# Kernel tuning notes

Hardware: AMD Instinct MI355X
Metric: run time of the kernel (lower is better)

## Reference

```python
import jax, jax.numpy as jnp
import numpy as np

CUTOFF = 8.0
NUM_RBF = 16
N = 2048
NUM_GRAPHS = 16


def setup_inputs() -> dict:
    key = jax.random.key(0)
    k1, k2 = jax.random.split(key)
    pos = jax.random.normal(k1, (N, 3), dtype=jnp.float32)
    batch = jnp.sort(jax.random.randint(k2, (N,), 0, NUM_GRAPHS)).astype(jnp.int64)
    # buffers from __init__
    centers = jnp.linspace(0.0, CUTOFF, NUM_RBF).astype(jnp.float32)
    width = jnp.asarray(CUTOFF / NUM_RBF * 0.5, dtype=jnp.float32)
    return {"pos": pos, "batch": batch, "centers": centers, "width": width}


def reference(pos, batch, centers, width):
    # Dense jit-friendly equivalent of the torch module: instead of filtering
    # pairs to a data-dependent edge list, we keep the full [N, N] pair grid
    # and return a boolean validity mask plus RBF features zeroed where invalid.
    n = pos.shape[0]
    idx = jnp.arange(n)
    diff = pos[:, None, :] - pos[None, :, :] + 1e-10  # [N, N, 3] (torch adds 1e-10 to diff)
    dist = jnp.sqrt(jnp.sum(diff * diff, axis=-1))     # [N, N]
    mask = (idx[:, None] != idx[None, :]) \
        & (batch[:, None] == batch[None, :]) \
        & (dist < CUTOFF)                               # [N, N] valid-edge mask
    # RBF encoding: exp(-(d - c)^2 / (2 w^2)), zeroed for invalid pairs
    rbf = jnp.exp(-((dist[..., None] - centers) ** 2) / (2.0 * width ** 2))  # [N, N, R]
    rbf = rbf * mask[..., None].astype(rbf.dtype)
    return mask, rbf
```

## Files before the change

### kernel.cpp

```cpp
#include <hip/hip_runtime.h>
#include <hip/hip_bf16.h>


constexpr int N     = 2048;
constexpr int NRBF  = 16;
constexpr int NTILE = N / 256;

typedef float  f32x4  __attribute__((ext_vector_type(4)));
typedef short  s16x8  __attribute__((ext_vector_type(8)));

__device__ inline float bf16_bits_to_f32(unsigned short h) {
    union { unsigned int u; float f; } c;
    c.u = ((unsigned int)h) << 16;
    return c.f;
}

__device__ inline short f32_to_bf16_bits(float f) {
    __hip_bfloat16 b = __float2bfloat16(f);
    union { __hip_bfloat16 b; short s; } c; c.b = b;
    return c.s;
}

__device__ inline float pair_dist(float xi, float yi, float zi,
                                  float xj, float yj, float zj) {
    const float dx = __fadd_rn(__fsub_rn(xi, xj), 1e-10f);
    const float dy = __fadd_rn(__fsub_rn(yi, yj), 1e-10f);
    const float dz = __fadd_rn(__fsub_rn(zi, zj), 1e-10f);
    const float d2 = __fadd_rn(__fadd_rn(__fmul_rn(dx, dx), __fmul_rn(dy, dy)),
                               __fmul_rn(dz, dz));
    return __fsqrt_rn(d2);
}

__global__ __launch_bounds__(256) void edge_rbf_kernel(
    const void* __restrict__ pos_raw,
    const int*  __restrict__ batch32,
    const void* __restrict__ centers_raw,
    const void* __restrict__ width_raw,
    void*       __restrict__ out_raw)
{
    const int lane = threadIdx.x & 63;
    const int wv   = threadIdx.x >> 6;
    const int i    = blockIdx.x;

    const unsigned int* posw = (const unsigned int*)pos_raw;
    int cnt = 0;
#pragma unroll
    for (int k = 0; k < 16; ++k) {
        float v = bf16_bits_to_f32((unsigned short)(posw[k] & 0xFFFFu));
        float a = fabsf(v);
        if (a > 1e-6f && a < 100.0f) ++cnt;
    }
    const bool is_bf16 = (cnt >= 12);
    const bool b64 = (batch32[N - 1] == 0);

    const int g = b64 ? batch32[2 * i] : batch32[i];
    int lo, hi;
    {
        int l = 0, h = N;
        while (l < h) {
            int m  = (l + h) >> 1;
            int bm = b64 ? batch32[2 * m] : batch32[m];
            if (bm < g) l = m + 1; else h = m;
        }
        lo = l;
        h = N;
        while (l < h) {
            int m  = (l + h) >> 1;
            int bm = b64 ? batch32[2 * m] : batch32[m];
            if (bm <= g) l = m + 1; else h = m;
        }
        hi = l;
    }

    const size_t row = (size_t)i * N;

    if (is_bf16) {
        const __hip_bfloat16* pos     = (const __hip_bfloat16*)pos_raw;
        const __hip_bfloat16* centers = (const __hip_bfloat16*)centers_raw;
        const __hip_bfloat16* width   = (const __hip_bfloat16*)width_raw;
        short* mask_out = (short*)out_raw;
        short* rbf_out  = mask_out + (size_t)N * N;

        const float xi = __bfloat162float(pos[3 * i + 0]);
        const float yi = __bfloat162float(pos[3 * i + 1]);
        const float zi = __bfloat162float(pos[3 * i + 2]);
        const float w  = __bfloat162float(width[0]);
        float cen[NRBF];
#pragma unroll
        for (int r = 0; r < NRBF; ++r) cen[r] = __bfloat162float(centers[r]);
        const float ninv = -1.0f / (2.0f * w * w);

        for (int t = 0; t < NTILE; ++t) {
            const int jt = t * 256 + wv * 64;
            const int jL = jt + lane;
            short* base = rbf_out + (row + jt) * NRBF;

            if (jt + 64 <= lo || jt >= hi) {
                mask_out[row + jL] = (short)0;
                s16x8 z = (s16x8)0;
#pragma unroll
                for (int q = 0; q < 2; ++q)
                    *(s16x8*)(base + q * 512 + lane * 8) = z;
                continue;
            }

            const bool eligL = (jL >= lo) && (jL < hi) && (jL != i);
            const float xjL = __bfloat162float(pos[3 * jL + 0]);
            const float yjL = __bfloat162float(pos[3 * jL + 1]);
            const float zjL = __bfloat162float(pos[3 * jL + 2]);
            const float dL  = pair_dist(xi, yi, zi, xjL, yjL, zjL);
            const bool validL = eligL && (dL < 8.0f);
            mask_out[row + jL] = f32_to_bf16_bits(validL ? 1.0f : 0.0f);

#pragma unroll
            for (int q = 0; q < 2; ++q) {
                const int p  = q * 32 + (lane >> 1);
                const int c0 = (lane & 1) * 8;
                const int jp = jt + p;
                const float xj = __bfloat162float(pos[3 * jp + 0]);
                const float yj = __bfloat162float(pos[3 * jp + 1]);
                const float zj = __bfloat162float(pos[3 * jp + 2]);
                const float d  = pair_dist(xi, yi, zi, xj, yj, zj);
                const bool  ok = (jp >= lo) && (jp < hi) && (jp != i)
                                 && (d < 8.0f);
                s16x8 o;
#pragma unroll
                for (int u = 0; u < 8; ++u) {
                    const float tt = d - cen[c0 + u];
                    o[u] = f32_to_bf16_bits(ok ? __expf(tt * tt * ninv) : 0.0f);
                }
                *(s16x8*)(base + q * 512 + lane * 8) = o;
            }
        }
    } else {
        const float* pos     = (const float*)pos_raw;
        const float* centers = (const float*)centers_raw;
        const float* width   = (const float*)width_raw;
        float* mask_out = (float*)out_raw;
        float* rbf_out  = mask_out + (size_t)N * N;

        const float xi = pos[3 * i + 0];
        const float yi = pos[3 * i + 1];
        const float zi = pos[3 * i + 2];
        const float w  = width[0];
        float cen[NRBF];
#pragma unroll
        for (int r = 0; r < NRBF; ++r) cen[r] = centers[r];
        const float ninv = -1.0f / (2.0f * w * w);

        for (int t = 0; t < NTILE; ++t) {
            const int jt = t * 256 + wv * 64;
            const int jL = jt + lane;
            float* base = rbf_out + (row + jt) * NRBF;

            if (jt + 64 <= lo || jt >= hi) {
                mask_out[row + jL] = 0.0f;
                f32x4 z = (f32x4)0.0f;
#pragma unroll
                for (int q = 0; q < 4; ++q)
                    *(f32x4*)(base + q * 256 + lane * 4) = z;
                continue;
            }

            const bool eligL = (jL >= lo) && (jL < hi) && (jL != i);
            const float xjL = pos[3 * jL + 0];
            const float yjL = pos[3 * jL + 1];
            const float zjL = pos[3 * jL + 2];
            const float dL  = pair_dist(xi, yi, zi, xjL, yjL, zjL);
            const bool validL = eligL && (dL < 8.0f);
            mask_out[row + jL] = validL ? 1.0f : 0.0f;

#pragma unroll
            for (int q = 0; q < 4; ++q) {
                const int p  = q * 16 + (lane >> 2);
                const int c0 = (lane & 3) * 4;
                const int jp = jt + p;
                const float xj = pos[3 * jp + 0];
                const float yj = pos[3 * jp + 1];
                const float zj = pos[3 * jp + 2];
                const float d  = pair_dist(xi, yi, zi, xj, yj, zj);
                const bool  ok = (jp >= lo) && (jp < hi) && (jp != i)
                                 && (d < 8.0f);
                f32x4 o;
#pragma unroll
                for (int u = 0; u < 4; ++u) {
                    const float tt = d - cen[c0 + u];
                    o[u] = ok ? __expf(tt * tt * ninv) : 0.0f;
                }
                *(f32x4*)(base + q * 256 + lane * 4) = o;
            }
        }
    }
}

extern "C" void kernel_launch(void* const* d_in, const int* in_sizes, int n_in,
                              void* d_out, int out_size, void* d_ws, size_t ws_size,
                              hipStream_t stream) {
    const void* pos     = d_in[0];
    const int*  batch   = (const int*)d_in[1];
    const void* centers = d_in[2];
    const void* width   = d_in[3];

    dim3 grid(N);
    dim3 block(256);
    edge_rbf_kernel<<<grid, block, 0, stream>>>(pos, batch, centers, width,
                                                d_out);
}
```

Baseline: 294.3 us.

## Precompute per-row graph ranges and switch to flat grid-stride output writes

Moves the per-row binary search over the batch array into a small separate kernel that writes lo/hi bounds to workspace. The main kernel becomes a fixed 512-block grid-stride loop where each thread writes contiguous 16-byte chunks of the rbf and mask outputs, so stores from consecutive threads are fully contiguous. The cost is an extra launch, per-element range loads, and recomputing the pair distance per chunk, and the block-level skip of tiles outside the row's graph is gone.

```diff
diff --git a/kernel.cpp b/kernel.cpp
--- a/kernel.cpp
+++ b/kernel.cpp
@@ -2,12 +2,14 @@
 #include <hip/hip_bf16.h>
 
 
-constexpr int N     = 2048;
-constexpr int NRBF  = 16;
-constexpr int NTILE = N / 256;
+constexpr int N    = 2048;
+constexpr int NRBF = 16;
+constexpr int NBLK = 512;
+constexpr int T    = NBLK * 256;
 
 typedef float  f32x4  __attribute__((ext_vector_type(4)));
 typedef short  s16x8  __attribute__((ext_vector_type(8)));
+typedef int    i32x2  __attribute__((ext_vector_type(2)));
 
 __device__ inline float bf16_bits_to_f32(unsigned short h) {
     union { unsigned int u; float f; } c;
@@ -31,16 +33,37 @@
     return __fsqrt_rn(d2);
 }
 
+__global__ __launch_bounds__(256) void row_range_kernel(
+    const int* __restrict__ batch32, int* __restrict__ ws)
+{
+    const int i = blockIdx.x * 256 + threadIdx.x;
+    const bool b64 = (batch32[N - 1] == 0);
+    const int g = b64 ? batch32[2 * i] : batch32[i];
+    int l = 0, h = N;
+    while (l < h) {
+        int m  = (l + h) >> 1;
+        int bm = b64 ? batch32[2 * m] : batch32[m];
+        if (bm < g) l = m + 1; else h = m;
+    }
+    const int lo = l;
+    h = N;
+    while (l < h) {
+        int m  = (l + h) >> 1;
+        int bm = b64 ? batch32[2 * m] : batch32[m];
+        if (bm <= g) l = m + 1; else h = m;
+    }
+    ws[2 * i]     = lo;
+    ws[2 * i + 1] = l;
+}
+
 __global__ __launch_bounds__(256) void edge_rbf_kernel(
     const void* __restrict__ pos_raw,
-    const int*  __restrict__ batch32,
     const void* __restrict__ centers_raw,
     const void* __restrict__ width_raw,
+    const int*  __restrict__ ws,
     void*       __restrict__ out_raw)
 {
-    const int lane = threadIdx.x & 63;
-    const int wv   = threadIdx.x >> 6;
-    const int i    = blockIdx.x;
+    const int g0 = blockIdx.x * 256 + threadIdx.x;
 
     const unsigned int* posw = (const unsigned int*)pos_raw;
     int cnt = 0;
@@ -51,144 +74,123 @@
         if (a > 1e-6f && a < 100.0f) ++cnt;
     }
     const bool is_bf16 = (cnt >= 12);
-    const bool b64 = (batch32[N - 1] == 0);
-
-    const int g = b64 ? batch32[2 * i] : batch32[i];
-    int lo, hi;
-    {
-        int l = 0, h = N;
-        while (l < h) {
-            int m  = (l + h) >> 1;
-            int bm = b64 ? batch32[2 * m] : batch32[m];
-            if (bm < g) l = m + 1; else h = m;
-        }
-        lo = l;
-        h = N;
-        while (l < h) {
-            int m  = (l + h) >> 1;
-            int bm = b64 ? batch32[2 * m] : batch32[m];
-            if (bm <= g) l = m + 1; else h = m;
-        }
-        hi = l;
-    }
-
-    const size_t row = (size_t)i * N;
-
-    if (is_bf16) {
+
+    if (!is_bf16) {
+        const float* pos     = (const float*)pos_raw;
+        const float* centers = (const float*)centers_raw;
+        const float* width   = (const float*)width_raw;
+        float* mask_out = (float*)out_raw;
+        float* rbf_out  = mask_out + (size_t)N * N;
+
+        const float w = width[0];
+        float cen[NRBF];
+#pragma unroll
+        for (int r = 0; r < NRBF; ++r) cen[r] = centers[r];
+        const float ninv = -1.0f / (2.0f * w * w);
+
+        for (int k = 0; k < 128; ++k) {
+            const int c    = g0 + k * T;
+            const int pidx = c >> 2;
+            const int q    = c & 3;
+            const int i    = pidx >> 11;
+            const int j    = pidx & (N - 1);
+            const i32x2 lh = *(const i32x2*)(ws + 2 * i);
+            f32x4 o = (f32x4)0.0f;
+            if ((j >= lh[0]) & (j < lh[1]) & (j != i)) {
+                const float d = pair_dist(pos[3*i], pos[3*i+1], pos[3*i+2],
+                                          pos[3*j], pos[3*j+1], pos[3*j+2]);
+                if (d < 8.0f) {
+#pragma unroll
+                    for (int u = 0; u < 4; ++u) {
+                        const float tt = d - cen[4 * q + u];
+                        o[u] = __expf(tt * tt * ninv);
+                    }
+                }
+            }
+            *(f32x4*)(rbf_out + (size_t)c * 4) = o;
+        }
+
+        for (int k = 0; k < 8; ++k) {
+            const int c  = g0 + k * T;
+            const int i  = c >> 9;
+            const int j0 = (c & 511) * 4;
+            const i32x2 lh = *(const i32x2*)(ws + 2 * i);
+            const float xi = pos[3*i], yi = pos[3*i+1], zi = pos[3*i+2];
+            f32x4 o;
+#pragma unroll
+            for (int m = 0; m < 4; ++m) {
+                const int j = j0 + m;
+                float v = 0.0f;
+                if ((j >= lh[0]) & (j < lh[1]) & (j != i)) {
+                    const float d = pair_dist(xi, yi, zi,
+                                              pos[3*j], pos[3*j+1], pos[3*j+2]);
+                    v = (d < 8.0f) ? 1.0f : 0.0f;
+                }
+                o[m] = v;
+            }
+            *(f32x4*)(mask_out + (size_t)c * 4) = o;
+        }
+    } else {
         const __hip_bfloat16* pos     = (const __hip_bfloat16*)pos_raw;
         const __hip_bfloat16* centers = (const __hip_bfloat16*)centers_raw;
         const __hip_bfloat16* width   = (const __hip_bfloat16*)width_raw;
         short* mask_out = (short*)out_raw;
         short* rbf_out  = mask_out + (size_t)N * N;
 
-        const float xi = __bfloat162float(pos[3 * i + 0]);
-        const float yi = __bfloat162float(pos[3 * i + 1]);
-        const float zi = __bfloat162float(pos[3 * i + 2]);
-        const float w  = __bfloat162float(width[0]);
+        const float w = __bfloat162float(width[0]);
         float cen[NRBF];
 #pragma unroll
         for (int r = 0; r < NRBF; ++r) cen[r] = __bfloat162float(centers[r]);
         const float ninv = -1.0f / (2.0f * w * w);
 
-        for (int t = 0; t < NTILE; ++t) {
-            const int jt = t * 256 + wv * 64;
-            const int jL = jt + lane;
-            short* base = rbf_out + (row + jt) * NRBF;
-
-            if (jt + 64 <= lo || jt >= hi) {
-                mask_out[row + jL] = (short)0;
-                s16x8 z = (s16x8)0;
-#pragma unroll
-                for (int q = 0; q < 2; ++q)
-                    *(s16x8*)(base + q * 512 + lane * 8) = z;
-                continue;
-            }
-
-            const bool eligL = (jL >= lo) && (jL < hi) && (jL != i);
-            const float xjL = __bfloat162float(pos[3 * jL + 0]);
-            const float yjL = __bfloat162float(pos[3 * jL + 1]);
-            const float zjL = __bfloat162float(pos[3 * jL + 2]);
-            const float dL  = pair_dist(xi, yi, zi, xjL, yjL, zjL);
-            const bool validL = eligL && (dL < 8.0f);
-            mask_out[row + jL] = f32_to_bf16_bits(validL ? 1.0f : 0.0f);
-
-#pragma unroll
-            for (int q = 0; q < 2; ++q) {
-                const int p  = q * 32 + (lane >> 1);
-                const int c0 = (lane & 1) * 8;
-                const int jp = jt + p;
-                const float xj = __bfloat162float(pos[3 * jp + 0]);
-                const float yj = __bfloat162float(pos[3 * jp + 1]);
-                const float zj = __bfloat162float(pos[3 * jp + 2]);
-                const float d  = pair_dist(xi, yi, zi, xj, yj, zj);
-                const bool  ok = (jp >= lo) && (jp < hi) && (jp != i)
-                                 && (d < 8.0f);
-                s16x8 o;
-#pragma unroll
-                for (int u = 0; u < 8; ++u) {
-                    const float tt = d - cen[c0 + u];
-                    o[u] = f32_to_bf16_bits(ok ? __expf(tt * tt * ninv) : 0.0f);
-                }
-                *(s16x8*)(base + q * 512 + lane * 8) = o;
-            }
-        }
-    } else {
-        const float* pos     = (const float*)pos_raw;
-        const float* centers = (const float*)centers_raw;
-        const float* width   = (const float*)width_raw;
-        float* mask_out = (float*)out_raw;
-        float* rbf_out  = mask_out + (size_t)N * N;
-
-        const float xi = pos[3 * i + 0];
-        const float yi = pos[3 * i + 1];
-        const float zi = pos[3 * i + 2];
-        const float w  = width[0];
-        float cen[NRBF];
-#pragma unroll
-        for (int r = 0; r < NRBF; ++r) cen[r] = centers[r];
-        const float ninv = -1.0f / (2.0f * w * w);
-
-        for (int t = 0; t < NTILE; ++t) {
-            const int jt = t * 256 + wv * 64;
-            const int jL = jt + lane;
-            float* base = rbf_out + (row + jt) * NRBF;
-
-            if (jt + 64 <= lo || jt >= hi) {
-                mask_out[row + jL] = 0.0f;
-                f32x4 z = (f32x4)0.0f;
-#pragma unroll
-                for (int q = 0; q < 4; ++q)
-                    *(f32x4*)(base + q * 256 + lane * 4) = z;
-                continue;
-            }
-
-            const bool eligL = (jL >= lo) && (jL < hi) && (jL != i);
-            const float xjL = pos[3 * jL + 0];
-            const float yjL = pos[3 * jL + 1];
-            const float zjL = pos[3 * jL + 2];
-            const float dL  = pair_dist(xi, yi, zi, xjL, yjL, zjL);
-            const bool validL = eligL && (dL < 8.0f);
-            mask_out[row + jL] = validL ? 1.0f : 0.0f;
-
-#pragma unroll
-            for (int q = 0; q < 4; ++q) {
-                const int p  = q * 16 + (lane >> 2);
-                const int c0 = (lane & 3) * 4;
-                const int jp = jt + p;
-                const float xj = pos[3 * jp + 0];
-                const float yj = pos[3 * jp + 1];
-                const float zj = pos[3 * jp + 2];
-                const float d  = pair_dist(xi, yi, zi, xj, yj, zj);
-                const bool  ok = (jp >= lo) && (jp < hi) && (jp != i)
-                                 && (d < 8.0f);
-                f32x4 o;
-#pragma unroll
-                for (int u = 0; u < 4; ++u) {
-                    const float tt = d - cen[c0 + u];
-                    o[u] = ok ? __expf(tt * tt * ninv) : 0.0f;
-                }
-                *(f32x4*)(base + q * 256 + lane * 4) = o;
-            }
+        for (int k = 0; k < 64; ++k) {
+            const int c    = g0 + k * T;
+            const int pidx = c >> 1;
+            const int h8   = (c & 1) * 8;
+            const int i    = pidx >> 11;
+            const int j    = pidx & (N - 1);
+            const i32x2 lh = *(const i32x2*)(ws + 2 * i);
+            s16x8 o = (s16x8)0;
+            if ((j >= lh[0]) & (j < lh[1]) & (j != i)) {
+                const float d = pair_dist(
+                    __bfloat162float(pos[3*i]),   __bfloat162float(pos[3*i+1]),
+                    __bfloat162float(pos[3*i+2]),
+                    __bfloat162float(pos[3*j]),   __bfloat162float(pos[3*j+1]),
+                    __bfloat162float(pos[3*j+2]));
+                if (d < 8.0f) {
+#pragma unroll
+                    for (int u = 0; u < 8; ++u) {
+                        const float tt = d - cen[h8 + u];
+                        o[u] = f32_to_bf16_bits(__expf(tt * tt * ninv));
+                    }
+                }
+            }
+            *(s16x8*)(rbf_out + (size_t)c * 8) = o;
+        }
+
+        for (int k = 0; k < 4; ++k) {
+            const int c  = g0 + k * T;
+            const int i  = c >> 8;
+            const int j0 = (c & 255) * 8;
+            const i32x2 lh = *(const i32x2*)(ws + 2 * i);
+            const float xi = __bfloat162float(pos[3*i]);
+            const float yi = __bfloat162float(pos[3*i+1]);
+            const float zi = __bfloat162float(pos[3*i+2]);
+            s16x8 o;
+#pragma unroll
+            for (int m = 0; m < 8; ++m) {
+                const int j = j0 + m;
+                float v = 0.0f;
+                if ((j >= lh[0]) & (j < lh[1]) & (j != i)) {
+                    const float d = pair_dist(
+                        xi, yi, zi,
+                        __bfloat162float(pos[3*j]), __bfloat162float(pos[3*j+1]),
+                        __bfloat162float(pos[3*j+2]));
+                    v = (d < 8.0f) ? 1.0f : 0.0f;
+                }
+                o[m] = f32_to_bf16_bits(v);
+            }
+            *(s16x8*)(mask_out + (size_t)c * 8) = o;
         }
     }
 }
@@ -201,8 +203,9 @@
     const void* centers = d_in[2];
     const void* width   = d_in[3];
 
-    dim3 grid(N);
-    dim3 block(256);
-    edge_rbf_kernel<<<grid, block, 0, stream>>>(pos, batch, centers, width,
-                                                d_out);
-}
+    row_range_kernel<<<dim3(N / 256), dim3(256), 0, stream>>>(
+        batch, (int*)d_ws);
+
+    edge_rbf_kernel<<<dim3(NBLK), dim3(256), 0, stream>>>(
+        pos, centers, width, (const int*)d_ws, d_out);
+}
```

After: 298.2 us, median of 2. No clear change (+1.3%).
